# Performance work log

Hardware: AMD Instinct MI355X
Metric: run time of the kernel (lower is better)

## Reference

```python
import jax, jax.numpy as jnp
import numpy as np
from jax import lax

EPS = 1e-5


def fps(xyz, npoint):
    # Farthest point sampling; xyz [B, N, 3] -> idx [B, npoint] (starts at point 0)
    B, N, _ = xyz.shape

    def body(carry, _):
        dist, far = carry
        c = jnp.take_along_axis(xyz, far[:, None, None], axis=1)  # [B,1,3]
        d = jnp.sum((xyz - c) ** 2, -1)                            # [B,N]
        dist = jnp.minimum(dist, d)
        nxt = jnp.argmax(dist, -1).astype(jnp.int32)
        return (dist, nxt), far

    init = (jnp.full((B, N), 1e10, xyz.dtype), jnp.zeros((B,), jnp.int32))
    _, idx = lax.scan(body, init, None, length=npoint)
    return idx.T  # [B, npoint]


def query_ball(radius, nsample, xyz, new_xyz):
    # xyz [B,N,3], new_xyz [B,S,3] -> idx [B,S,nsample]
    N = xyz.shape[1]
    sqr = jnp.sum((new_xyz[:, :, None, :] - xyz[:, None, :, :]) ** 2, -1)  # [B,S,N]
    idx = jnp.where(sqr > radius * radius, N, jnp.arange(N)[None, None, :])
    idx = jnp.sort(idx, axis=-1)[:, :, :nsample]
    # out-of-ball slots get replaced by the first in-ball index (torch repo behavior)
    return jnp.where(idx == N, idx[:, :, :1], idx)


def gather_pts(x, idx):
    # x [B,N,C], idx [B,...] -> [B,...,C]
    B = x.shape[0]
    b = jnp.arange(B).reshape((B,) + (1,) * (idx.ndim - 1))
    return x[b, idx]


def mlp_bn(x, layers):
    # x [B,S,K,C]; shared 1x1-conv MLP + training-mode BatchNorm + ReLU
    for w, g, b in layers:
        x = jnp.einsum('bskc,oc->bsko', x, w)
        mean = x.mean((0, 1, 2))
        var = x.var((0, 1, 2))  # biased, as torch BN uses for normalization
        x = jax.nn.relu((x - mean) * lax.rsqrt(var + EPS) * g + b)
    return x


def set_abstraction(xyz, points, npoint, radius, nsample, layers, group_all):
    B = xyz.shape[0]
    if group_all:
        new_xyz = jnp.zeros((B, 1, 3), xyz.dtype)
        new_points = xyz[:, None]  # [B,1,N,3] (raw xyz, no centering)
        if points is not None:
            new_points = jnp.concatenate([new_points, points[:, None]], -1)
    else:
        fidx = fps(xyz, npoint)
        new_xyz = gather_pts(xyz, fidx)                     # [B,S,3]
        idx = query_ball(radius, nsample, xyz, new_xyz)     # [B,S,K]
        grouped = gather_pts(xyz, idx) - new_xyz[:, :, None, :]
        if points is not None:
            new_points = jnp.concatenate([grouped, gather_pts(points, idx)], -1)
        else:
            new_points = grouped
    feat = mlp_bn(new_points, layers).max(2)  # max-pool over neighbors -> [B,S,C]
    return new_xyz, feat


def _forward(xyz_time, l1, l2, l3):
    B, T, N, _ = xyz_time.shape
    x = xyz_time.reshape(B * T, N, 4)
    xyz, t = x[..., :3], x[..., 3:]
    x1_xyz, x1 = set_abstraction(xyz, t, 512, 0.2, 32, l1, False)
    x2_xyz, x2 = set_abstraction(x1_xyz, x1, 128, 0.4, 64, l2, False)
    _, x3 = set_abstraction(x2_xyz, x2, None, None, None, l3, True)
    return x3.reshape(B, T, -1)


def setup_inputs() -> dict:
    key = jax.random.key(0)
    ks = jax.random.split(key, 16)
    inp = {"xyz_time": jax.random.uniform(ks[0], (2, 4, 4096, 4), jnp.float32)}
    specs = {1: [(64, 4), (64, 64), (128, 64)],
             2: [(128, 131), (128, 128), (256, 128)],
             3: [(256, 259), (512, 256), (1024, 512)]}
    i = 1
    for s, layers in specs.items():
        for j, (o, c) in enumerate(layers):
            inp[f"w{s}_{j}"] = jax.random.normal(jax.random.fold_in(ks[i], j), (o, c), jnp.float32) * 0.1
            inp[f"g{s}_{j}"] = jnp.ones((o,), jnp.float32)
            inp[f"b{s}_{j}"] = jnp.zeros((o,), jnp.float32)
        i += 1
    return inp


def reference(xyz_time, w1_0, g1_0, b1_0, w1_1, g1_1, b1_1, w1_2, g1_2, b1_2,
              w2_0, g2_0, b2_0, w2_1, g2_1, b2_1, w2_2, g2_2, b2_2,
              w3_0, g3_0, b3_0, w3_1, g3_1, b3_1, w3_2, g3_2, b3_2):
    l1 = [(w1_0, g1_0, b1_0), (w1_1, g1_1, b1_1), (w1_2, g1_2, b1_2)]
    l2 = [(w2_0, g2_0, b2_0), (w2_1, g2_1, b2_1), (w2_2, g2_2, b2_2)]
    l3 = [(w3_0, g3_0, b3_0), (w3_1, g3_1, b3_1), (w3_2, g3_2, b3_2)]
    return _forward(xyz_time, l1, l2, l3)
```

## Files before the change

kernel.cpp:

```cpp
#include <hip/hip_runtime.h>


typedef short s16x8 __attribute__((ext_vector_type(8)));
typedef float f32x4 __attribute__((ext_vector_type(4)));

__device__ __forceinline__ unsigned short f2bf_rne(float f) {
    unsigned u = __float_as_uint(f);
    u += 0x7FFFu + ((u >> 16) & 1u);
    return (unsigned short)(u >> 16);
}
__device__ __forceinline__ void f2bf_split(float v, unsigned short& hi,
                                           unsigned short& lo) {
    unsigned u = __float_as_uint(v);
    unsigned r = u + 0x7FFFu + ((u >> 16) & 1u);
    hi = (unsigned short)(r >> 16);
    float vh = __uint_as_float(r & 0xFFFF0000u);
    lo = f2bf_rne(v - vh);
}

__device__ __forceinline__ unsigned long long umax64(unsigned long long a,
                                                     unsigned long long b) {
    return a > b ? a : b;
}

__device__ __forceinline__ unsigned wred_umax63(unsigned v) {
    unsigned t;
    t = (unsigned)__builtin_amdgcn_update_dpp(0, (int)v, 0x111, 0xf, 0xf, true); if (t > v) v = t;
    t = (unsigned)__builtin_amdgcn_update_dpp(0, (int)v, 0x112, 0xf, 0xf, true); if (t > v) v = t;
    t = (unsigned)__builtin_amdgcn_update_dpp(0, (int)v, 0x114, 0xf, 0xf, true); if (t > v) v = t;
    t = (unsigned)__builtin_amdgcn_update_dpp(0, (int)v, 0x118, 0xf, 0xf, true); if (t > v) v = t;
    t = (unsigned)__builtin_amdgcn_update_dpp(0, (int)v, 0x142, 0xa, 0xf, true); if (t > v) v = t;
    t = (unsigned)__builtin_amdgcn_update_dpp(0, (int)v, 0x143, 0xc, 0xf, true); if (t > v) v = t;
    return v;
}

__device__ __forceinline__ void wave_argmax(unsigned dbits, unsigned nInv,
                                            unsigned& vmax, unsigned& iInv) {
    unsigned m = wred_umax63(dbits);
    vmax = (unsigned)__builtin_amdgcn_readlane((int)m, 63);
    unsigned cand = (dbits == vmax) ? nInv : 0u;
    unsigned im = wred_umax63(cand);
    iInv = (unsigned)__builtin_amdgcn_readlane((int)im, 63);
}

struct PWArgs {
    const float* w[9];
    unsigned off[9];
    int O[9], C[9], CP[9];
};
__device__ __forceinline__ void prep_w_dev(const PWArgs& a,
                                           unsigned short* __restrict__ wh,
                                           unsigned short* __restrict__ wl,
                                           int i) {
    int l = 0;
#pragma unroll
    for (int k = 1; k < 9; ++k) if (i >= (int)a.off[k]) l = k;
    int li = i - (int)a.off[l];
    int CP = a.CP[l];
    int o = li / CP;
    int c = li - o * CP;
    float v = (c < a.C[l]) ? a.w[l][(size_t)o * a.C[l] + c] : 0.f;
    unsigned short h, lo;
    f2bf_split(v, h, lo);
    wh[i] = h; wl[i] = lo;
}

template<int NT, int ITEMS, int STRIDE>
__global__ __launch_bounds__(NT) void fps_block(
    const float* __restrict__ pts, int npoint,
    int* __restrict__ outIdx, float* __restrict__ outXyz,
    int nFps, PWArgs pw, unsigned short* __restrict__ wh,
    unsigned short* __restrict__ wl, int wtotal)
{
    constexpr int N = NT * ITEMS;
    constexpr int NW = NT / 64;
    __shared__ float4 scoord[N];
    __shared__ unsigned long long wkey[2][NW];

    if (blockIdx.x >= nFps) {
        int i = (blockIdx.x - nFps) * NT + threadIdx.x;
        if (i < wtotal) prep_w_dev(pw, wh, wl, i);
        return;
    }

    const int b = blockIdx.x;
    const int tid = threadIdx.x;
    const int wid = tid >> 6;
    const int lane = tid & 63;
    const float* P = pts + (size_t)b * N * STRIDE;

    float px[ITEMS], py[ITEMS], pz[ITEMS], dloc[ITEMS];
#pragma unroll
    for (int w = 0; w < ITEMS; ++w) {
        int n = tid + w * NT;
        float x, y, z;
        if (STRIDE == 4) {
            float4 v = *(const float4*)(P + (size_t)n * 4);
            x = v.x; y = v.y; z = v.z;
        } else {
            x = P[(size_t)n * STRIDE + 0];
            y = P[(size_t)n * STRIDE + 1];
            z = P[(size_t)n * STRIDE + 2];
        }
        px[w] = x; py[w] = y; pz[w] = z;
        scoord[n] = make_float4(x, y, z, 0.f);
        dloc[w] = 1e10f;
    }
    __syncthreads();
    float4 c0 = scoord[0];
    float cx = c0.x, cy = c0.y, cz = c0.z;
    int far = 0;

    for (int i = 0; i < npoint; ++i) {
        if (tid == 0) {
            outIdx[(size_t)b * npoint + i] = far;
            outXyz[((size_t)b * npoint + i) * 3 + 0] = cx;
            outXyz[((size_t)b * npoint + i) * 3 + 1] = cy;
            outXyz[((size_t)b * npoint + i) * 3 + 2] = cz;
        }
        float bestV = -1.0f;
        int bestW = 0;
#pragma unroll
        for (int w = 0; w < ITEMS; ++w) {
            float dx = __fsub_rn(px[w], cx);
            float dy = __fsub_rn(py[w], cy);
            float dz = __fsub_rn(pz[w], cz);
            float d = __fadd_rn(__fadd_rn(__fmul_rn(dx, dx), __fmul_rn(dy, dy)),
                                __fmul_rn(dz, dz));
            float dd = fminf(dloc[w], d);
            dloc[w] = dd;
            if (dd > bestV) { bestV = dd; bestW = w; }
        }
        int bestN = tid + bestW * NT;
        unsigned vmax, iInv;
        wave_argmax(__float_as_uint(bestV), 0xFFFFFFFFu ^ (unsigned)bestN,
                    vmax, iInv);
        const int par = i & 1;
        if (lane == 0)
            wkey[par][wid] = ((unsigned long long)vmax << 32) | iInv;
        __syncthreads();
        unsigned long long kb = wkey[par][0];
#pragma unroll
        for (int w2 = 1; w2 < NW; ++w2) kb = umax64(kb, wkey[par][w2]);
        far = (int)(0xFFFFFFFFu ^ (unsigned)kb);
        float4 cc = scoord[far];
        cx = cc.x; cy = cc.y; cz = cc.z;
    }
}

__device__ void fps_wave_dev(const float* __restrict__ pts, int npoint,
                             int* __restrict__ outIdx, float* __restrict__ outXyz,
                             int b, float4* scoord)
{
    constexpr int ITEMS = 8;
    constexpr int STRIDE = 3;
    constexpr int N = 64 * ITEMS;
    const int tid = threadIdx.x;
    const float* P = pts + (size_t)b * N * STRIDE;

    float px[ITEMS], py[ITEMS], pz[ITEMS], dloc[ITEMS];
#pragma unroll
    for (int w = 0; w < ITEMS; ++w) {
        int n = tid + w * 64;
        float x = P[(size_t)n * STRIDE + 0];
        float y = P[(size_t)n * STRIDE + 1];
        float z = P[(size_t)n * STRIDE + 2];
        px[w] = x; py[w] = y; pz[w] = z;
        scoord[n] = make_float4(x, y, z, 0.f);
        dloc[w] = 1e10f;
    }
    __threadfence_block();
    float4 c0 = scoord[0];
    float cx = c0.x, cy = c0.y, cz = c0.z;
    int far = 0;

    for (int i = 0; i < npoint; ++i) {
        if (tid == 0) {
            outIdx[(size_t)b * npoint + i] = far;
            outXyz[((size_t)b * npoint + i) * 3 + 0] = cx;
            outXyz[((size_t)b * npoint + i) * 3 + 1] = cy;
            outXyz[((size_t)b * npoint + i) * 3 + 2] = cz;
        }
        float bestV = -1.0f;
        int bestW = 0;
#pragma unroll
        for (int w = 0; w < ITEMS; ++w) {
            float dx = __fsub_rn(px[w], cx);
            float dy = __fsub_rn(py[w], cy);
            float dz = __fsub_rn(pz[w], cz);
            float d = __fadd_rn(__fadd_rn(__fmul_rn(dx, dx), __fmul_rn(dy, dy)),
                                __fmul_rn(dz, dz));
            float dd = fminf(dloc[w], d);
            dloc[w] = dd;
            if (dd > bestV) { bestV = dd; bestW = w; }
        }
        int bestN = tid + bestW * 64;
        unsigned vmax, iInv;
        wave_argmax(__float_as_uint(bestV), 0xFFFFFFFFu ^ (unsigned)bestN,
                    vmax, iInv);
        far = (int)(0xFFFFFFFFu ^ iInv);
        float4 cc = scoord[far];
        cx = cc.x; cy = cc.y; cz = cc.z;
    }
}

__global__ __launch_bounds__(256) void qb_group1(
    const float* __restrict__ xyz ,
    const float* __restrict__ ctr ,
    float* __restrict__ out ,
    int nQb, const float* __restrict__ fpsPts,
    int* __restrict__ fpsIdx, float* __restrict__ fpsXyz)
{
    __shared__ float4 scoord[512];
    if ((int)blockIdx.x >= nQb) {
        if (threadIdx.x < 64)
            fps_wave_dev(fpsPts, 128, fpsIdx, fpsXyz,
                         (int)blockIdx.x - nQb, scoord);
        return;
    }
    int gw = (blockIdx.x * 256 + threadIdx.x) >> 6;
    int lane = threadIdx.x & 63;
    if (gw >= 4096) return;
    int b = gw >> 9;
    const float* P = xyz + (size_t)b * 4096 * 4;
    float cx = ctr[(size_t)gw * 3 + 0];
    float cy = ctr[(size_t)gw * 3 + 1];
    float cz = ctr[(size_t)gw * 3 + 2];
    float* out0 = out + (size_t)gw * 32 * 8;
    int cnt = 0;
    float f0x = 0.f, f0y = 0.f, f0z = 0.f, f0t = 0.f;
    bool haveFirst = false;
    for (int base = 0; base < 4096 && cnt < 32; base += 64) {
        int n = base + lane;
        float4 p = *(const float4*)(P + (size_t)n * 4);
        float ex = __fsub_rn(p.x, cx);
        float ey = __fsub_rn(p.y, cy);
        float ez = __fsub_rn(p.z, cz);
        float d = __fadd_rn(__fadd_rn(__fmul_rn(ex, ex), __fmul_rn(ey, ey)),
                            __fmul_rn(ez, ez));
        bool inb = !(d > 0.04f);
        unsigned long long mask = __ballot(inb);
        if (mask) {
            if (!haveFirst) {
                int fl = (int)__builtin_ctzll(mask);
                f0x = __shfl(ex, fl); f0y = __shfl(ey, fl);
                f0z = __shfl(ez, fl); f0t = __shfl(p.w, fl);
                haveFirst = true;
            }
            if (inb) {
                int pos = cnt + __builtin_popcountll(mask & ((1ull << lane) - 1ull));
                if (pos < 32) {
                    float* o = out0 + (size_t)pos * 8;
                    *(float4*)o = make_float4(ex, ey, ez, p.w);
                    *(float4*)(o + 4) = make_float4(0.f, 0.f, 0.f, 0.f);
                }
            }
            cnt += (int)__builtin_popcountll(mask);
        }
    }
    if (cnt > 32) cnt = 32;
    for (int p2 = cnt + lane; p2 < 32; p2 += 64) {
        float* o = out0 + (size_t)p2 * 8;
        *(float4*)o = make_float4(f0x, f0y, f0z, f0t);
        *(float4*)(o + 4) = make_float4(0.f, 0.f, 0.f, 0.f);
    }
}

__device__ __forceinline__ void qb2_dev(
    const float* __restrict__ xyz, const float* __restrict__ centers,
    int* __restrict__ outIdx, int gw, int lane)
{
    const int N = 512, stride = 3, S = 128, nsample = 64;
    const float r2 = 0.16f;
    int b = gw / S;
    const float* P = xyz + (size_t)b * N * stride;
    float cx = centers[(size_t)gw * 3 + 0];
    float cy = centers[(size_t)gw * 3 + 1];
    float cz = centers[(size_t)gw * 3 + 2];
    int* out = outIdx + (size_t)gw * nsample;
    int cnt = 0;
    int firstIdx = 0;
    bool haveFirst = false;
    for (int base = 0; base < N && cnt < nsample; base += 64) {
        int n = base + lane;
        bool inb = false;
        if (n < N) {
            float dx = __fsub_rn(cx, P[(size_t)n * stride + 0]);
            float dy = __fsub_rn(cy, P[(size_t)n * stride + 1]);
            float dz = __fsub_rn(cz, P[(size_t)n * stride + 2]);
            float d = __fadd_rn(__fadd_rn(__fmul_rn(dx, dx), __fmul_rn(dy, dy)),
                                __fmul_rn(dz, dz));
            inb = !(d > r2);
        }
        unsigned long long mask = __ballot(inb);
        if (mask) {
            if (!haveFirst) { firstIdx = base + __builtin_ctzll(mask); haveFirst = true; }
            if (inb) {
                int pos = cnt + __builtin_popcountll(mask & ((1ull << lane) - 1ull));
                if (pos < nsample) out[pos] = n;
            }
            cnt += (int)__builtin_popcountll(mask);
        }
    }
    if (cnt > nsample) cnt = nsample;
    for (int p = cnt + lane; p < nsample; p += 64) out[p] = firstIdx;
}

__global__ __launch_bounds__(256) void gemm_fused(
    const float* __restrict__ X,
    const double* __restrict__ pSin, const double* __restrict__ pQin,
    const float* __restrict__ gIn, const float* __restrict__ bIn,
    double invMin, int applyAct,
    const unsigned short* __restrict__ Bh, const unsigned short* __restrict__ Bl,
    float* __restrict__ Y,
    double* __restrict__ pSout, double* __restrict__ pQout,
    int AC, int CPW, int O, int gmode,
    const int* __restrict__ gqb, const float* __restrict__ gxyz,
    const float* __restrict__ gctr, const float* __restrict__ gfeat,
    int redK, float* __restrict__ Vmax, float* __restrict__ Vmin)
{
    constexpr int PITCH = 40;
    __shared__ __align__(16) unsigned short sAh[128 * PITCH];
    __shared__ __align__(16) unsigned short sAl[128 * PITCH];
    __shared__ __align__(16) unsigned short sBh[128 * PITCH];
    __shared__ __align__(16) unsigned short sBl[128 * PITCH];
    __shared__ float sred[2048];
    __shared__ float sScale[512];
    __shared__ float sShift[512];

    const int tid = threadIdx.x;
    const int lane = tid & 63;
    const int wid = tid >> 6;
    const int col15 = lane & 15;
    const int quad = lane >> 4;
    const int wm = (wid >> 1) * 64;
    const int wo = (wid & 1) * 64;
    const int m0 = blockIdx.x * 128;
    const int o0 = blockIdx.y * 128;
    const int lr = tid >> 2;
    const int lc = (tid & 3) * 8;

    if (applyAct) {
        for (int c = tid; c < AC; c += 256) {
            double S = pSin[c], Q = pQin[c];
            double mean = S * invMin;
            double var = Q * invMin - mean * mean;
            float varf = (float)var;
            if (varf < 0.f) varf = 0.f;
            float sc = gIn[c] * rsqrtf(varf + 1e-5f);
            sScale[c] = sc;
            sShift[c] = bIn[c] - (float)mean * sc;
        }
    }
    __syncthreads();

    f32x4 acc[4][4];
#pragma unroll
    for (int mt = 0; mt < 4; ++mt)
#pragma unroll
        for (int ot = 0; ot < 4; ++ot)
            acc[mt][ot] = {0.f, 0.f, 0.f, 0.f};

    for (int k0 = 0; k0 < CPW; k0 += 32) {
#pragma unroll
        for (int it = 0; it < 2; ++it) {
            int r = lr + it * 64;
            int c = k0 + lc;
            unsigned short h[8], l[8];
            float vv[8];
            bool have = true;
            if (gmode == 0) {
                if (c + 8 <= AC) {
                    const float* xr = X + (size_t)(m0 + r) * AC + c;
                    float4 v0 = *(const float4*)xr;
                    float4 v1 = *(const float4*)(xr + 4);
                    vv[0] = v0.x; vv[1] = v0.y; vv[2] = v0.z; vv[3] = v0.w;
                    vv[4] = v1.x; vv[5] = v1.y; vv[6] = v1.z; vv[7] = v1.w;
                    if (applyAct) {
#pragma unroll
                        for (int j = 0; j < 8; ++j)
                            vv[j] = fmaxf(vv[j] * sScale[c + j] + sShift[c + j], 0.f);
                    }
                } else {
                    have = false;
                }
            } else if (gmode == 2) {
                int m = m0 + r;
                int idx = gqb[m];
                idx = (idx < 0) ? 0 : (idx > 511 ? 511 : idx);
                int bb2 = m >> 13;
                int bs = m >> 6;
                const float* frow = gfeat + ((size_t)bb2 * 512 + idx) * 128;
                const float* xrow = gxyz + ((size_t)bb2 * 512 + idx) * 3;
                const float* crow = gctr + (size_t)bs * 3;
#pragma unroll
                for (int j = 0; j < 8; ++j) {
                    int cc = c + j;
                    float v = 0.f;
                    if (cc < 3)        v = __fsub_rn(xrow[cc], crow[cc]);
                    else if (cc < 131) v = frow[cc - 3];
                    vv[j] = v;
                }
            } else {
                int m = m0 + r;
                const float* frow = gfeat + (size_t)m * 256;
                const float* crow = gctr + (size_t)m * 3;
#pragma unroll
                for (int j = 0; j < 8; ++j) {
                    int cc = c + j;
                    float v = 0.f;
                    if (cc < 3)        v = crow[cc];
                    else if (cc < 259) v = frow[cc - 3];
                    vv[j] = v;
                }
            }
            if (have) {
#pragma unroll
                for (int j = 0; j < 8; ++j) f2bf_split(vv[j], h[j], l[j]);
            } else {
#pragma unroll
                for (int j = 0; j < 8; ++j) { h[j] = 0; l[j] = 0; }
            }
            *(ushort4*)&sAh[r * PITCH + lc] = make_ushort4(h[0], h[1], h[2], h[3]);
            *(ushort4*)&sAh[r * PITCH + lc + 4] = make_ushort4(h[4], h[5], h[6], h[7]);
            *(ushort4*)&sAl[r * PITCH + lc] = make_ushort4(l[0], l[1], l[2], l[3]);
            *(ushort4*)&sAl[r * PITCH + lc + 4] = make_ushort4(l[4], l[5], l[6], l[7]);
        }
#pragma unroll
        for (int it = 0; it < 2; ++it) {
            int r = lr + it * 64;
            int c = k0 + lc;
            int o = o0 + r;
            uint4 vh = {0, 0, 0, 0}, vl = {0, 0, 0, 0};
            if (o < O && c < CPW) {
                size_t goff = (size_t)o * CPW + c;
                vh = *(const uint4*)(Bh + goff);
                vl = *(const uint4*)(Bl + goff);
            }
            *(uint4*)&sBh[r * PITCH + lc] = vh;
            *(uint4*)&sBl[r * PITCH + lc] = vl;
        }
        __syncthreads();
        s16x8 ah[4], al[4], bh[4], bl[4];
#pragma unroll
        for (int mt = 0; mt < 4; ++mt) {
            int rowoff = (wm + mt * 16 + col15) * PITCH + quad * 8;
            ah[mt] = *(const s16x8*)&sAh[rowoff];
            al[mt] = *(const s16x8*)&sAl[rowoff];
        }
#pragma unroll
        for (int ot = 0; ot < 4; ++ot) {
            int rowoff = (wo + ot * 16 + col15) * PITCH + quad * 8;
            bh[ot] = *(const s16x8*)&sBh[rowoff];
            bl[ot] = *(const s16x8*)&sBl[rowoff];
        }
#pragma unroll
        for (int mt = 0; mt < 4; ++mt)
#pragma unroll
            for (int ot = 0; ot < 4; ++ot) {
                acc[mt][ot] = __builtin_amdgcn_mfma_f32_16x16x32_bf16(
                    ah[mt], bl[ot], acc[mt][ot], 0, 0, 0);
                acc[mt][ot] = __builtin_amdgcn_mfma_f32_16x16x32_bf16(
                    al[mt], bh[ot], acc[mt][ot], 0, 0, 0);
                acc[mt][ot] = __builtin_amdgcn_mfma_f32_16x16x32_bf16(
                    ah[mt], bh[ot], acc[mt][ot], 0, 0, 0);
            }
        __syncthreads();
    }
    if (redK == 0) {
#pragma unroll
        for (int mt = 0; mt < 4; ++mt)
#pragma unroll
            for (int ot = 0; ot < 4; ++ot) {
                int og = o0 + wo + ot * 16 + col15;
                if (og < O) {
#pragma unroll
                    for (int r = 0; r < 4; ++r) {
                        int mg = m0 + wm + mt * 16 + quad * 4 + r;
                        Y[(size_t)mg * O + og] = acc[mt][ot][r];
                    }
                }
            }
    } else if (redK == 32) {
#pragma unroll
        for (int ot = 0; ot < 4; ++ot) {
            int og = o0 + wo + ot * 16 + col15;
#pragma unroll
            for (int cp = 0; cp < 2; ++cp) {
                float mx = acc[2 * cp][ot][0];
                float mn = mx;
#pragma unroll
                for (int mi = 0; mi < 2; ++mi)
#pragma unroll
                    for (int r = 0; r < 4; ++r) {
                        float v = acc[2 * cp + mi][ot][r];
                        mx = fmaxf(mx, v);
                        mn = fminf(mn, v);
                    }
                mx = fmaxf(mx, __shfl_xor(mx, 16));
                mx = fmaxf(mx, __shfl_xor(mx, 32));
                mn = fminf(mn, __shfl_xor(mn, 16));
                mn = fminf(mn, __shfl_xor(mn, 32));
                if (quad == 0) {
                    int ctr = (m0 >> 5) + (wm >> 5) + cp;
                    Vmax[(size_t)ctr * O + og] = mx;
                    Vmin[(size_t)ctr * O + og] = mn;
                }
            }
        }
    } else {
#pragma unroll
        for (int ot = 0; ot < 4; ++ot) {
            int og = o0 + wo + ot * 16 + col15;
            float mx = acc[0][ot][0];
            float mn = mx;
#pragma unroll
            for (int mt = 0; mt < 4; ++mt)
#pragma unroll
                for (int r = 0; r < 4; ++r) {
                    float v = acc[mt][ot][r];
                    mx = fmaxf(mx, v);
                    mn = fminf(mn, v);
                }
            mx = fmaxf(mx, __shfl_xor(mx, 16));
            mx = fmaxf(mx, __shfl_xor(mx, 32));
            mn = fminf(mn, __shfl_xor(mn, 16));
            mn = fminf(mn, __shfl_xor(mn, 32));
            if (quad == 0) {
                int ctr = (m0 >> 6) + (wm >> 6);
                Vmax[(size_t)ctr * O + og] = mx;
                Vmin[(size_t)ctr * O + og] = mn;
            }
        }
    }
#pragma unroll
    for (int ot = 0; ot < 4; ++ot) {
        float s = 0.f, s2 = 0.f;
#pragma unroll
        for (int mt = 0; mt < 4; ++mt)
#pragma unroll
            for (int r = 0; r < 4; ++r) {
                float v = acc[mt][ot][r];
                s += v;
                s2 += v * v;
            }
        int slot = ((wid * 4 + quad) * 16 + col15) * 4 + ot;
        sred[slot * 2] = s;
        sred[slot * 2 + 1] = s2;
    }
    __syncthreads();
    if (tid < 128) {
        int col = tid;
        int o = o0 + col;
        if (o < O) {
            int cb = col >> 6;
            int ot = (col & 63) >> 4;
            int c15 = col & 15;
            double S = 0.0, S2 = 0.0;
#pragma unroll
            for (int wp = 0; wp < 2; ++wp) {
                int wd = cb + wp * 2;
#pragma unroll
                for (int q = 0; q < 4; ++q) {
                    int slot = ((wd * 4 + q) * 16 + c15) * 4 + ot;
                    S += (double)sred[slot * 2];
                    S2 += (double)sred[slot * 2 + 1];
                }
            }
            atomicAdd(&pSout[o], S);
            atomicAdd(&pQout[o], S2);
        }
    }
}

__global__ __launch_bounds__(256) void bn_relu_max(
    const float* __restrict__ Y, const float* __restrict__ Vmin,
    const double* __restrict__ pS, const double* __restrict__ pQ,
    const float* __restrict__ gv, const float* __restrict__ bv, double invM,
    float* __restrict__ out, int Stot, int K, int O, int vmode, int nMain,
    const float* __restrict__ qbXyz, const float* __restrict__ qbCtr,
    int* __restrict__ qbOut)
{
    if ((int)blockIdx.x >= nMain) {
        int wid = threadIdx.x >> 6, lane = threadIdx.x & 63;
        int gw = ((int)blockIdx.x - nMain) * 4 + wid;
        if (gw < 1024) qb2_dev(qbXyz, qbCtr, qbOut, gw, lane);
        return;
    }
    int idx = blockIdx.x * 256 + threadIdx.x;
    if (idx >= Stot * O) return;
    int s = idx / O;
    int o = idx - s * O;
    double S = pS[o], Q = pQ[o];
    double mean = S * invM;
    double var = Q * invM - mean * mean;
    float varf = (float)var;
    if (varf < 0.f) varf = 0.f;
    float sc = gv[o] * rsqrtf(varf + 1e-5f);
    float sh = bv[o] - (float)mean * sc;
    if (vmode) {
        float vmax = Y[(size_t)s * O + o];
        float vmin = Vmin[(size_t)s * O + o];
        float v = (sc >= 0.f) ? vmax : vmin;
        out[idx] = fmaxf(v * sc + sh, 0.f);
        return;
    }
    const float* basep = Y + (size_t)s * K * O + o;
    float mx = 0.f;
    for (int k = 0; k < K; ++k) {
        float v = basep[(size_t)k * O] * sc + sh;
        v = fmaxf(v, 0.f);
        mx = fmaxf(mx, v);
    }
    out[idx] = mx;
}

extern "C" void kernel_launch(void* const* d_in, const int* in_sizes, int n_in,
                              void* d_out, int out_size, void* d_ws, size_t ws_size,
                              hipStream_t stream)
{
    const float* xin = (const float*)d_in[0];
    const float* w[9]; const float* g[9]; const float* bb[9];
    for (int i = 0; i < 9; ++i) {
        w[i]  = (const float*)d_in[1 + 3 * i];
        g[i]  = (const float*)d_in[2 + 3 * i];
        bb[i] = (const float*)d_in[3 + 3 * i];
    }

    char* base = (char*)d_ws;
    size_t off = 0;
    auto alloc = [&](size_t bytes) -> void* {
        void* p = base + off;
        off = (off + bytes + 255) & ~(size_t)255;
        return p;
    };
    const int OC[9][3] = {{64,4,8},{64,64,64},{128,64,64},
                          {128,131,136},{128,128,128},{256,128,128},
                          {256,259,264},{512,256,256},{1024,512,512}};
    size_t woff[10]; woff[0] = 0;
    for (int i = 0; i < 9; ++i) woff[i + 1] = woff[i] + (size_t)OC[i][0] * OC[i][2];

    int*    fps1   = (int*)alloc((size_t)4096 * 4);
    int*    fps2   = (int*)alloc((size_t)1024 * 4);
    int*    qb2    = (int*)alloc((size_t)65536 * 4);
    float*  nx1    = (float*)alloc((size_t)12288 * 4);
    float*  nx2    = (float*)alloc((size_t)3072 * 4);
    float*  feat1  = (float*)alloc((size_t)524288 * 4);
    float*  feat2  = (float*)alloc((size_t)262144 * 4);
    double* partS  = (double*)alloc((size_t)9 * 1024 * 8);
    double* partQ  = (double*)alloc((size_t)9 * 1024 * 8);
    unsigned short* WH = (unsigned short*)alloc(woff[9] * 2);
    unsigned short* WL = (unsigned short*)alloc(woff[9] * 2);
    const size_t zeroBytes = off;
    float*  XG = (float*)alloc((size_t)65536 * 136 * 4);
    float*  A  = (float*)alloc((size_t)16777216 * 4);
    if (off > ws_size) return;

    hipMemsetAsync(d_ws, 0, zeroBytes, stream);

    PWArgs pwa;
    for (int i = 0; i < 9; ++i) {
        pwa.w[i] = w[i]; pwa.off[i] = (unsigned)woff[i];
        pwa.O[i] = OC[i][0]; pwa.C[i] = OC[i][1]; pwa.CP[i] = OC[i][2];
    }
    const int nPrep = (int)((woff[9] + 255) / 256);

    auto gemm = [&](const float* X, int prevLi, double invMprev, int li,
                    float* Y, int YB, int OB, int AC, int CPW, int O,
                    int gmode, const int* gqb, const float* gxyz,
                    const float* gctr, const float* gfeat,
                    int redK, float* Vmax, float* Vmin) {
        gemm_fused<<<dim3(YB, OB), 256, 0, stream>>>(
            X,
            prevLi >= 0 ? partS + (size_t)prevLi * 1024 : nullptr,
            prevLi >= 0 ? partQ + (size_t)prevLi * 1024 : nullptr,
            prevLi >= 0 ? g[prevLi] : nullptr,
            prevLi >= 0 ? bb[prevLi] : nullptr,
            invMprev, prevLi >= 0 ? 1 : 0,
            WH + woff[li], WL + woff[li], Y,
            partS + (size_t)li * 1024, partQ + (size_t)li * 1024,
            AC, CPW, O, gmode, gqb, gxyz, gctr, gfeat, redK, Vmax, Vmin);
    };

    const double inv1 = 1.0 / 131072.0;
    const double inv2 = 1.0 / 65536.0;
    const double inv3 = 1.0 / 1024.0;

    fps_block<256, 16, 4><<<8 + nPrep, 256, 0, stream>>>(
        xin, 512, fps1, nx1, 8, pwa, WH, WL, (int)woff[9]);
    qb_group1<<<1024 + 8, 256, 0, stream>>>(xin, nx1, XG, 1024, nx1, fps2, nx2);

    gemm(XG, -1, 0.0, 0, A, 1024, 1, 8, 8, 64, 0, nullptr, nullptr, nullptr, nullptr, 0, nullptr, nullptr);
    gemm(A, 0, inv1, 1, XG, 1024, 1, 64, 64, 64, 0, nullptr, nullptr, nullptr, nullptr, 0, nullptr, nullptr);
    gemm(XG, 1, inv1, 2, A, 1024, 1, 64, 64, 128, 0, nullptr, nullptr, nullptr, nullptr, 32, A, A + 524288);
    bn_relu_max<<<2048 + 256, 256, 0, stream>>>(
        A, A + 524288, partS + 2 * 1024, partQ + 2 * 1024, g[2], bb[2], inv1,
        feat1, 4096, 32, 128, 1, 2048, nx1, nx2, qb2);

    gemm(nullptr, -1, 0.0, 3, A, 512, 1, 136, 136, 128, 2, qb2, nx1, nx2, feat1, 0, nullptr, nullptr);
    gemm(A, 3, inv2, 4, XG, 512, 1, 128, 128, 128, 0, nullptr, nullptr, nullptr, nullptr, 0, nullptr, nullptr);
    gemm(XG, 4, inv2, 5, A, 512, 2, 128, 128, 256, 0, nullptr, nullptr, nullptr, nullptr, 64, A, A + 262144);
    bn_relu_max<<<(1024 * 256) / 256, 256, 0, stream>>>(
        A, A + 262144, partS + 5 * 1024, partQ + 5 * 1024, g[5], bb[5], inv2,
        feat2, 1024, 64, 256, 1, 1024 * 256 / 256, nullptr, nullptr, nullptr);

    gemm(nullptr, -1, 0.0, 6, A, 8, 2, 264, 264, 256, 3, nullptr, nullptr, nx2, feat2, 0, nullptr, nullptr);
    gemm(A, 6, inv3, 7, XG, 8, 4, 256, 256, 512, 0, nullptr, nullptr, nullptr, nullptr, 0, nullptr, nullptr);
    gemm(XG, 7, inv3, 8, A, 8, 8, 512, 512, 1024, 0, nullptr, nullptr, nullptr, nullptr, 0, nullptr, nullptr);
    bn_relu_max<<<(8 * 1024) / 256, 256, 0, stream>>>(
        A, nullptr, partS + 8 * 1024, partQ + 8 * 1024, g[8], bb[8], inv3,
        (float*)d_out, 8, 128, 1024, 0, (8 * 1024) / 256,
        nullptr, nullptr, nullptr);
}
```

Measured before the change: 794.8 us.

## Fuse first MLP layer and BN statistics into ball-query grouping kernel

```diff
diff --git a/kernel.cpp b/kernel.cpp
--- a/kernel.cpp
+++ b/kernel.cpp
@@ -207,26 +207,30 @@
 __global__ __launch_bounds__(256) void qb_group1(
     const float* __restrict__ xyz ,
     const float* __restrict__ ctr ,
-    float* __restrict__ out ,
+    const float* __restrict__ W0 ,
+    float* __restrict__ Yout ,
+    double* __restrict__ pS0, double* __restrict__ pQ0,
     int nQb, const float* __restrict__ fpsPts,
     int* __restrict__ fpsIdx, float* __restrict__ fpsXyz)
 {
     __shared__ float4 scoord[512];
+    __shared__ float4 srows[4][32];
+    __shared__ float sstat[4][64][2];
     if ((int)blockIdx.x >= nQb) {
         if (threadIdx.x < 64)
             fps_wave_dev(fpsPts, 128, fpsIdx, fpsXyz,
                          (int)blockIdx.x - nQb, scoord);
         return;
     }
-    int gw = (blockIdx.x * 256 + threadIdx.x) >> 6;
-    int lane = threadIdx.x & 63;
-    if (gw >= 4096) return;
+    const int tid = threadIdx.x;
+    const int gw = (blockIdx.x * 256 + tid) >> 6;
+    const int wid = tid >> 6;
+    const int lane = tid & 63;
     int b = gw >> 9;
     const float* P = xyz + (size_t)b * 4096 * 4;
     float cx = ctr[(size_t)gw * 3 + 0];
     float cy = ctr[(size_t)gw * 3 + 1];
     float cz = ctr[(size_t)gw * 3 + 2];
-    float* out0 = out + (size_t)gw * 32 * 8;
     int cnt = 0;
     float f0x = 0.f, f0y = 0.f, f0z = 0.f, f0t = 0.f;
     bool haveFirst = false;
@@ -249,20 +253,43 @@
             }
             if (inb) {
                 int pos = cnt + __builtin_popcountll(mask & ((1ull << lane) - 1ull));
-                if (pos < 32) {
-                    float* o = out0 + (size_t)pos * 8;
-                    *(float4*)o = make_float4(ex, ey, ez, p.w);
-                    *(float4*)(o + 4) = make_float4(0.f, 0.f, 0.f, 0.f);
-                }
+                if (pos < 32)
+                    srows[wid][pos] = make_float4(ex, ey, ez, p.w);
             }
             cnt += (int)__builtin_popcountll(mask);
         }
     }
     if (cnt > 32) cnt = 32;
-    for (int p2 = cnt + lane; p2 < 32; p2 += 64) {
-        float* o = out0 + (size_t)p2 * 8;
-        *(float4*)o = make_float4(f0x, f0y, f0z, f0t);
-        *(float4*)(o + 4) = make_float4(0.f, 0.f, 0.f, 0.f);
+    for (int p2 = cnt + lane; p2 < 32; p2 += 64)
+        srows[wid][p2] = make_float4(f0x, f0y, f0z, f0t);
+    __syncthreads();
+
+    float wc0 = W0[lane * 4 + 0];
+    float wc1 = W0[lane * 4 + 1];
+    float wc2 = W0[lane * 4 + 2];
+    float wc3 = W0[lane * 4 + 3];
+    float s = 0.f, s2 = 0.f;
+    float* yp = Yout + (size_t)gw * 32 * 64 + lane;
+#pragma unroll 4
+    for (int r = 0; r < 32; ++r) {
+        float4 e = srows[wid][r];
+        float y = e.x * wc0 + e.y * wc1 + e.z * wc2 + e.w * wc3;
+        yp[(size_t)r * 64] = y;
+        s += y;
+        s2 += y * y;
+    }
+    sstat[wid][lane][0] = s;
+    sstat[wid][lane][1] = s2;
+    __syncthreads();
+    if (tid < 64) {
+        double S = 0.0, S2 = 0.0;
+#pragma unroll
+        for (int w2 = 0; w2 < 4; ++w2) {
+            S += (double)sstat[w2][tid][0];
+            S2 += (double)sstat[w2][tid][1];
+        }
+        atomicAdd(&pS0[tid], S);
+        atomicAdd(&pQ0[tid], S2);
     }
 }
 
@@ -688,20 +715,20 @@
 
     fps_block<256, 16, 4><<<8 + nPrep, 256, 0, stream>>>(
         xin, 512, fps1, nx1, 8, pwa, WH, WL, (int)woff[9]);
-    qb_group1<<<1024 + 8, 256, 0, stream>>>(xin, nx1, XG, 1024, nx1, fps2, nx2);
-
-    gemm(XG, -1, 0.0, 0, A, 1024, 1, 8, 8, 64, 0, nullptr, nullptr, nullptr, nullptr, 0, nullptr, nullptr);
+    qb_group1<<<1024 + 8, 256, 0, stream>>>(
+        xin, nx1, w[0], A, partS + 0, partQ + 0, 1024, nx1, fps2, nx2);
+
     gemm(A, 0, inv1, 1, XG, 1024, 1, 64, 64, 64, 0, nullptr, nullptr, nullptr, nullptr, 0, nullptr, nullptr);
     gemm(XG, 1, inv1, 2, A, 1024, 1, 64, 64, 128, 0, nullptr, nullptr, nullptr, nullptr, 32, A, A + 524288);
     bn_relu_max<<<2048 + 256, 256, 0, stream>>>(
         A, A + 524288, partS + 2 * 1024, partQ + 2 * 1024, g[2], bb[2], inv1,
         feat1, 4096, 32, 128, 1, 2048, nx1, nx2, qb2);
 
-    gemm(nullptr, -1, 0.0, 3, A, 512, 1, 136, 136, 128, 2, qb2, nx1, nx2, feat1, 0, nullptr, nullptr);
-    gemm(A, 3, inv2, 4, XG, 512, 1, 128, 128, 128, 0, nullptr, nullptr, nullptr, nullptr, 0, nullptr, nullptr);
-    gemm(XG, 4, inv2, 5, A, 512, 2, 128, 128, 256, 0, nullptr, nullptr, nullptr, nullptr, 64, A, A + 262144);
+    gemm(nullptr, -1, 0.0, 3, XG, 512, 1, 136, 136, 128, 2, qb2, nx1, nx2, feat1, 0, nullptr, nullptr);
+    gemm(XG, 3, inv2, 4, A, 512, 1, 128, 128, 128, 0, nullptr, nullptr, nullptr, nullptr, 0, nullptr, nullptr);
+    gemm(A, 4, inv2, 5, XG, 512, 2, 128, 128, 256, 0, nullptr, nullptr, nullptr, nullptr, 64, XG, XG + 262144);
     bn_relu_max<<<(1024 * 256) / 256, 256, 0, stream>>>(
-        A, A + 262144, partS + 5 * 1024, partQ + 5 * 1024, g[5], bb[5], inv2,
+        XG, XG + 262144, partS + 5 * 1024, partQ + 5 * 1024, g[5], bb[5], inv2,
         feat2, 1024, 64, 256, 1, 1024 * 256 / 256, nullptr, nullptr, nullptr);
 
     gemm(nullptr, -1, 0.0, 6, A, 8, 2, 264, 264, 256, 3, nullptr, nullptr, nx2, feat2, 0, nullptr, nullptr);
```

After: 767.0 us. 3.5% less time.
